# Kernel tuning notes

Hardware: AMD Instinct MI355X
Metric: run time of the kernel (lower is better)

The kernel has to match this reference:

```python
import jax, jax.numpy as jnp
import numpy as np
import math

DIMS, HEAD = 1024, 16
HD = DIMS // HEAD          # 64
B, CTX = 4, 1024
MAX_ITER, THRESH = 3, 0.5  # temp=1.0 -> q temperature scaling branch is skipped (as in torch)
LOG10_21 = math.log10(1.0 + 4000.0 / 200.0)


def _freq_angles(c):
    # compute_freqs_base: 0.2*(10**linspace(0, log10(21), d/2) - 1), custom_freqs = 36000/220 * base
    d2 = HD // 2
    mel = 10.0 ** jnp.linspace(0.0, LOG10_21, d2) - 1.0
    freqs = (36000.0 / 220.0) * (200.0 * mel / 1000.0)        # [d2]
    t = jnp.arange(c, dtype=jnp.float32)
    return t[:, None] * freqs[None, :]                          # [c, d2]


def _rope(x, ang):
    # lucidrains rotary_embedding_torch convention: interleaved pairs (x0,x1),(x2,x3),...
    x1, x2 = x[..., 0::2], x[..., 1::2]
    cos, sin = jnp.cos(ang), jnp.sin(ang)
    out = jnp.stack([x1 * cos - x2 * sin, x1 * sin + x2 * cos], axis=-1)
    return out.reshape(x.shape)


def _rms(x, w):
    eps = jnp.finfo(x.dtype).eps  # torch nn.RMSNorm eps=None default
    return x * jax.lax.rsqrt(jnp.mean(jnp.square(x), -1, keepdims=True) + eps) * w


def _sdpa(q, k, v):
    # mask is always None in this module's forward -> non-causal SDPA
    s = jnp.einsum('bhqd,bhkd->bhqk', q, k) / math.sqrt(q.shape[-1])
    return jnp.einsum('bhqk,bhkd->bhqd', jax.nn.softmax(s, -1), v)


def _focus(x, xa, P):
    # x: [b, cq, D] queries, xa: [b, ck, D] keys/values. In our configs cq == ck == eff_span.
    b, cq, D = x.shape
    ck = xa.shape[1]
    q = _rms(x, P['wq_norm']) @ P['Wq'] + P['bq']
    q = q.reshape(b, cq, HEAD, HD).transpose(0, 2, 1, 3)                 # b h c d
    kv = _rms(xa, P['wkv_norm']) @ P['Wkv'] + P['bkv']
    kv = kv.reshape(b, ck, 2, HEAD, HD).transpose(2, 0, 3, 1, 4)         # kv b h c d
    k, v = kv[0], kv[1]
    q = _rope(q, _freq_angles(cq))
    k = _rope(k, _freq_angles(ck))

    e = min(cq, ck)  # static; equals cq in all call sites here
    curq, kc, vc = q, k[:, :, :e], v[:, :, :e]
    prev = jnp.zeros_like(q)
    attn_out = jnp.zeros_like(q)
    done = jnp.asarray(False)
    for it in range(MAX_ITER):
        # torch: q/k/v re-projected from current state EVERY iteration (k,v compound)
        qp = curq[:, :, :e] @ P['Wlq'] + P['blq']
        kp = kc @ P['Wlk'] + P['blk']
        vp = vc @ P['Wlv'] + P['blv']
        attn = _sdpa(_rms(qp, P['wln']), _rms(kp, P['wln']), vp)         # == iter_out since e == cq
        diff = jnp.mean(jnp.abs(attn - prev))
        stop = (diff < THRESH) & (it > 0) & (~done)
        attn_out = jnp.where(done, attn_out, attn)  # on the break iteration attn_out = iter_out
        done = done | stop
        curq = jnp.where(done, curq, curq + attn)
        prev = jnp.where(done, prev, attn)
        kc = jnp.where(done, kc, kp)
        vc = jnp.where(done, vc, vp)
    return attn_out.transpose(0, 2, 1, 3).reshape(b, cq, D)             # b c (h d)


def _slide(x, P):
    # win_size = head_dim; only the first win_size keys of each span are ever used
    b, ctx, D = x.shape
    w = HD
    off = w // HEAD                       # span_len - win_size
    nwin = ctx // w                       # ctx chosen as a multiple of w
    starts = jnp.maximum(jnp.arange(nwin) * w - off, 0)
    kidx = starts[:, None] + jnp.arange(w)[None, :]                      # [nwin, w]
    qwin = x.reshape(b, nwin, w, D).transpose(1, 0, 2, 3)                # [nwin, b, w, D]
    kwin = x[:, kidx, :].transpose(1, 0, 2, 3)                           # [nwin, b, w, D]
    outw = jax.vmap(lambda xq, xk: _focus(xq, xk, P))(qwin, kwin)
    return outw.transpose(1, 0, 2, 3).reshape(b, ctx, D)


def _forward(x, xa, P):
    xw = _slide(x, P)
    xaw = _slide(xa, P)
    out = _focus(xw, xaw, P)
    return out @ P['Wo'] + P['bo']        # Dropout(0.01) is identity in eval


def setup_inputs() -> dict:
    key = jax.random.key(0)
    ks = jax.random.split(key, 8)
    s = 0.02
    f32 = jnp.float32
    return {
        'x': jax.random.normal(ks[0], (B, CTX, DIMS), f32),
        'xa': jax.random.normal(ks[1], (B, CTX, DIMS), f32),
        'wq_norm': jnp.ones((DIMS,), f32),
        'Wq': jax.random.normal(ks[2], (DIMS, DIMS), f32) * s,
        'bq': jnp.zeros((DIMS,), f32),
        'wkv_norm': jnp.ones((DIMS,), f32),
        'Wkv': jax.random.normal(ks[3], (DIMS, 2 * DIMS), f32) * s,
        'bkv': jnp.zeros((2 * DIMS,), f32),
        'wln': jnp.ones((HD,), f32),
        'Wlq': jax.random.normal(ks[4], (HD, HD), f32) * s,
        'blq': jnp.zeros((HD,), f32),
        'Wlk': jax.random.normal(ks[5], (HD, HD), f32) * s,
        'blk': jnp.zeros((HD,), f32),
        'Wlv': jax.random.normal(ks[6], (HD, HD), f32) * s,
        'blv': jnp.zeros((HD,), f32),
        'Wo': jax.random.normal(ks[7], (DIMS, DIMS), f32) * s,
        'bo': jnp.zeros((DIMS,), f32),
    }


def reference(x, xa, wq_norm, Wq, bq, wkv_norm, Wkv, bkv, wln, Wlq, blq, Wlk, blk, Wlv, blv, Wo, bo):
    P = dict(wq_norm=wq_norm, Wq=Wq, bq=bq, wkv_norm=wkv_norm, Wkv=Wkv, bkv=bkv, wln=wln,
             Wlq=Wlq, blq=blq, Wlk=Wlk, blk=blk, Wlv=Wlv, blv=blv, Wo=Wo, bo=bo)
    return _forward(x, xa, P)
```

## Files before the change

kernel.cpp:

```cpp
#include <hip/hip_runtime.h>
#include <math.h>

#define TPB 256

static __device__ __forceinline__ float4 mk4(float a, float b, float c, float d) {
  float4 r; r.x = a; r.y = b; r.z = c; r.w = d; return r;
}

__global__ __launch_bounds__(TPB) void k_tables(float* __restrict__ cosb,
                                                float* __restrict__ sinb) {
  int gid = blockIdx.x * TPB + threadIdx.x;
  if (gid >= 1024 * 32) return;
  int t = gid >> 5, j = gid & 31;
  const double Ld = 1.3222192947339193;
  float Lf = (float)Ld;
  float mlog;
  if (j == 31) {
    mlog = Lf;
  } else {
    float stepf = (float)((double)j / 31.0);
    mlog = (float)((double)Lf * (double)stepf);
  }
  float p = (float)pow(10.0, (double)mlog);
  float mel = p - 1.0f;
  float t2 = (200.0f * mel) / 1000.0f;
  float freq = 163.63636363636363f * t2;
  float ang = (float)t * freq;
  double a = (double)ang;
  cosb[gid] = (float)cos(a);
  sinb[gid] = (float)sin(a);
}

__global__ __launch_bounds__(TPB) void k_rowinv(const float* __restrict__ X,
                                                float* __restrict__ inv) {
  __shared__ float red[4];
  int row = blockIdx.x;
  int tid = threadIdx.x;
  float4 v = *(const float4*)(X + (size_t)row * 1024 + tid * 4);
  float ss = v.x * v.x + v.y * v.y + v.z * v.z + v.w * v.w;
#pragma unroll
  for (int m = 1; m < 64; m <<= 1) ss += __shfl_xor(ss, m);
  if ((tid & 63) == 0) red[tid >> 6] = ss;
  __syncthreads();
  if (tid == 0) {
    float s = ((red[0] + red[1]) + (red[2] + red[3]));
    float mm = s * (1.0f / 1024.0f) + 1.1920928955078125e-7f;
    inv[row] = (float)(1.0 / sqrt((double)mm));
  }
}

__global__ __launch_bounds__(TPB) void k_gemm128(
    const float* __restrict__ X, const float* __restrict__ inv,
    const float* __restrict__ wn, const float* __restrict__ W,
    const float* __restrict__ bias, float* __restrict__ o0,
    float* __restrict__ o1, int N, int mode) {
  __shared__ float As[16][132];
  __shared__ float Bs[16][132];
  int tid = threadIdx.x;
  int bx = blockIdx.x, by = blockIdx.y;
  int tx = tid & 15, ty = tid >> 4;
  float c[8][8];
#pragma unroll
  for (int i = 0; i < 8; ++i)
#pragma unroll
    for (int j = 0; j < 8; ++j) c[i][j] = 0.0f;

  int arow = tid >> 1;
  float sA = 1.0f;
  if (inv) sA = inv[by * 128 + arow];
  const float* Xrow = X + (size_t)(by * 128 + arow) * 1024;

  for (int k0 = 0; k0 < 1024; k0 += 16) {
#pragma unroll
    for (int u = 0; u < 2; ++u) {
      int kq = ((tid & 1) * 2 + u) * 4;
      float4 a4 = *(const float4*)(Xrow + k0 + kq);
      if (wn) {
        float4 w4 = *(const float4*)(wn + k0 + kq);
        a4.x *= w4.x; a4.y *= w4.y; a4.z *= w4.z; a4.w *= w4.w;
      }
      a4.x *= sA; a4.y *= sA; a4.z *= sA; a4.w *= sA;
      As[kq + 0][arow] = a4.x;
      As[kq + 1][arow] = a4.y;
      As[kq + 2][arow] = a4.z;
      As[kq + 3][arow] = a4.w;
    }
#pragma unroll
    for (int u = 0; u < 2; ++u) {
      int kr = tid >> 4;
      int c4 = ((tid & 15) * 2 + u) * 4;
      *(float4*)&Bs[kr][c4] =
          *(const float4*)(W + (size_t)(k0 + kr) * N + bx * 128 + c4);
    }
    __syncthreads();
#pragma unroll
    for (int kk = 0; kk < 16; ++kk) {
      float4 a0 = *(const float4*)&As[kk][ty * 4];
      float4 a1 = *(const float4*)&As[kk][64 + ty * 4];
      float4 b0 = *(const float4*)&Bs[kk][tx * 4];
      float4 b1 = *(const float4*)&Bs[kk][64 + tx * 4];
      float av[8] = {a0.x, a0.y, a0.z, a0.w, a1.x, a1.y, a1.z, a1.w};
      float bv[8] = {b0.x, b0.y, b0.z, b0.w, b1.x, b1.y, b1.z, b1.w};
#pragma unroll
      for (int i = 0; i < 8; ++i)
#pragma unroll
        for (int j = 0; j < 8; ++j) c[i][j] += av[i] * bv[j];
    }
    __syncthreads();
  }

#pragma unroll
  for (int jh = 0; jh < 2; ++jh) {
    int colbase = bx * 128 + jh * 64 + tx * 4;
    float4 bb = {0.f, 0.f, 0.f, 0.f};
    if (bias) bb = *(const float4*)(bias + colbase);
#pragma unroll
    for (int ih = 0; ih < 2; ++ih) {
#pragma unroll
      for (int i2 = 0; i2 < 4; ++i2) {
        int row = by * 128 + ih * 64 + ty * 4 + i2;
        int ci = ih * 4 + i2;
        float4 o;
        o.x = c[ci][jh * 4 + 0] + bb.x;
        o.y = c[ci][jh * 4 + 1] + bb.y;
        o.z = c[ci][jh * 4 + 2] + bb.z;
        o.w = c[ci][jh * 4 + 3] + bb.w;
        if (mode == 0) {
          *(float4*)(o0 + (size_t)row * N + colbase) = o;
        } else {
          int b = row >> 10, t = row & 1023;
          float* dst = o0;
          int cc = colbase;
          if (mode == 2 && colbase >= 1024) { dst = o1; cc = colbase - 1024; }
          int ch = cc >> 6, d = cc & 63;
          *(float4*)(dst + ((size_t)((b * 16 + ch) * 1024 + t)) * 64 + d) = o;
        }
      }
    }
  }
}

__global__ __launch_bounds__(TPB) void k_rope(float* __restrict__ A, int mask,
                                              const float* __restrict__ cosb,
                                              const float* __restrict__ sinb) {
  int gid = blockIdx.x * TPB + threadIdx.x;
  int j = gid & 31;
  int row = gid >> 5;
  int t = row & 1023;
  int aidx = ((t & mask) << 5) + j;
  float cc = cosb[aidx], sn = sinb[aidx];
  size_t base = (size_t)row * 64;
  float x1 = A[base + 2 * j], x2 = A[base + 2 * j + 1];
  A[base + 2 * j] = x1 * cc - x2 * sn;
  A[base + 2 * j + 1] = x1 * sn + x2 * cc;
}

__global__ __launch_bounds__(TPB) void k_gather(
    const float* __restrict__ K, const float* __restrict__ V,
    float* __restrict__ kc, float* __restrict__ vc,
    const float* __restrict__ cosb, const float* __restrict__ sinb) {
  int gid = blockIdx.x * TPB + threadIdx.x;
  int j = gid & 31;
  int tl = (gid >> 5) & 63;
  int win = (gid >> 11) & 15;
  int h = (gid >> 15) & 15;
  int b = gid >> 19;
  int sw = win * 64 - 4;
  if (win == 0) sw = 0;
  size_t bh = (size_t)(b * 16 + h) * 1024;
  size_t src = (bh + sw + tl) * 64;
  size_t dst = (bh + win * 64 + tl) * 64;
  int aidx = (tl << 5) + j;
  float cc = cosb[aidx], sn = sinb[aidx];
  float k1 = K[src + 2 * j], k2 = K[src + 2 * j + 1];
  kc[dst + 2 * j] = k1 * cc - k2 * sn;
  kc[dst + 2 * j + 1] = k1 * sn + k2 * cc;
  vc[dst + 2 * j] = V[src + 2 * j];
  vc[dst + 2 * j + 1] = V[src + 2 * j + 1];
}

__global__ __launch_bounds__(TPB) void k_proj(
    const float* __restrict__ curq, float* __restrict__ kc,
    float* __restrict__ vc, float* __restrict__ qph, float* __restrict__ kphT,
    const float* __restrict__ Wlq, const float* __restrict__ blq,
    const float* __restrict__ Wlk, const float* __restrict__ blk,
    const float* __restrict__ Wlv, const float* __restrict__ blv,
    const float* __restrict__ wln, int CQ, const int* __restrict__ flags) {
  int RT = CQ >> 4;
  int bid = blockIdx.x;
  int rt = bid % RT;
  int rest = bid / RT;
  int h = rest & 15; rest >>= 4;
  int b = rest & 3;
  int win = rest >> 2;
  if (flags && flags[win]) return;
  __shared__ float qs[16][68], ksm[16][68], vsm[16][68];
  __shared__ float Wqs[4096], Wks[4096], Wvs[4096];
  int tid = threadIdx.x;
#pragma unroll
  for (int i = 0; i < 4; ++i) {
    int f4 = (i * 256 + tid) * 4;
    *(float4*)&Wqs[f4] = *(const float4*)(Wlq + f4);
    *(float4*)&Wks[f4] = *(const float4*)(Wlk + f4);
    *(float4*)&Wvs[f4] = *(const float4*)(Wlv + f4);
  }
  int lr = tid >> 4, c4 = (tid & 15) * 4;
  int bh = b * 16 + h;
  size_t rowbase = (size_t)bh * 1024 + (size_t)win * CQ + rt * 16;
  size_t g = (rowbase + lr) * 64 + c4;
  *(float4*)&qs[lr][c4] = *(const float4*)(curq + g);
  *(float4*)&ksm[lr][c4] = *(const float4*)(kc + g);
  *(float4*)&vsm[lr][c4] = *(const float4*)(vc + g);
  __syncthreads();
  int r = tid >> 4, cg = tid & 15;
  int tglob = win * CQ + rt * 16 + r;
  const float eps = 1.1920928955078125e-7f;
  float4 wl4 = *(const float4*)(wln + cg * 4);
  size_t orow = (rowbase + r) * 64 + cg * 4;
  float4 acc;
  float ssum, rms;
  acc = *(const float4*)(blq + cg * 4);
#pragma unroll 8
  for (int k = 0; k < 64; ++k) {
    float xv = qs[r][k];
    float4 w4 = *(const float4*)&Wqs[k * 64 + cg * 4];
    acc.x += xv * w4.x; acc.y += xv * w4.y;
    acc.z += xv * w4.z; acc.w += xv * w4.w;
  }
  ssum = acc.x * acc.x + acc.y * acc.y + acc.z * acc.z + acc.w * acc.w;
#pragma unroll
  for (int m = 1; m < 16; m <<= 1) ssum += __shfl_xor(ssum, m);
  rms = (float)(1.0 / sqrt((double)(ssum * 0.015625f + eps)));
  {
    float4 o;
    o.x = acc.x * rms * wl4.x; o.y = acc.y * rms * wl4.y;
    o.z = acc.z * rms * wl4.z; o.w = acc.w * rms * wl4.w;
    *(float4*)(qph + orow) = o;
  }
  acc = *(const float4*)(blk + cg * 4);
#pragma unroll 8
  for (int k = 0; k < 64; ++k) {
    float xv = ksm[r][k];
    float4 w4 = *(const float4*)&Wks[k * 64 + cg * 4];
    acc.x += xv * w4.x; acc.y += xv * w4.y;
    acc.z += xv * w4.z; acc.w += xv * w4.w;
  }
  *(float4*)(kc + orow) = acc;
  ssum = acc.x * acc.x + acc.y * acc.y + acc.z * acc.z + acc.w * acc.w;
#pragma unroll
  for (int m = 1; m < 16; m <<= 1) ssum += __shfl_xor(ssum, m);
  rms = (float)(1.0 / sqrt((double)(ssum * 0.015625f + eps)));
  {
    float no0 = acc.x * rms * wl4.x;
    float no1 = acc.y * rms * wl4.y;
    float no2 = acc.z * rms * wl4.z;
    float no3 = acc.w * rms * wl4.w;
    size_t tb = (size_t)bh * 64 + cg * 4;
    kphT[(tb + 0) * 1024 + tglob] = no0;
    kphT[(tb + 1) * 1024 + tglob] = no1;
    kphT[(tb + 2) * 1024 + tglob] = no2;
    kphT[(tb + 3) * 1024 + tglob] = no3;
  }
  acc = *(const float4*)(blv + cg * 4);
#pragma unroll 8
  for (int k = 0; k < 64; ++k) {
    float xv = vsm[r][k];
    float4 w4 = *(const float4*)&Wvs[k * 64 + cg * 4];
    acc.x += xv * w4.x; acc.y += xv * w4.y;
    acc.z += xv * w4.z; acc.w += xv * w4.w;
  }
  *(float4*)(vc + orow) = acc;
}

template <int FRAG>
__global__ __launch_bounds__(TPB, 2) void k_attn_t(
    const float* __restrict__ qph, const float* __restrict__ kphT,
    const float* __restrict__ vbuf, float* __restrict__ curq,
    float* __restrict__ prevb, float* __restrict__ outb,
    float* __restrict__ diffp, const int* __restrict__ flags, int NQT,
    int nt, int mode) {
  constexpr int QT = FRAG * 16;
  int bid = blockIdx.x;
  int qt = bid % NQT;
  int bh = bid / NQT;
  int h = bh & 15, b = bh >> 4;
  if (mode == 2 && flags[(nt == 1) ? qt : 0]) return;
  __shared__ float qTs[64][QT];
  __shared__ float kps[64 * QT];
  __shared__ float vss[64 * 64];
  int tid = threadIdx.x;
  int tx = tid & 15, ty = tid >> 4;
  size_t bh1024 = (size_t)bh * 1024;
  size_t bh64 = (size_t)bh * 64;
  int q0 = qt * QT;
#pragma unroll
  for (int i = 0; i < FRAG; ++i) {
    int f4id = i * 256 + tid;
    int row = f4id >> 4;
    int c4 = (f4id & 15) * 4;
    float4 v = *(const float4*)(qph + (bh1024 + q0 + row) * 64 + c4);
    qTs[c4 + 0][row] = v.x;
    qTs[c4 + 1][row] = v.y;
    qTs[c4 + 2][row] = v.z;
    qTs[c4 + 3][row] = v.w;
  }
  float m[FRAG], l[FRAG], acc[FRAG][4];
#pragma unroll
  for (int i = 0; i < FRAG; ++i) {
    m[i] = -INFINITY; l[i] = 0.0f;
    acc[i][0] = acc[i][1] = acc[i][2] = acc[i][3] = 0.0f;
  }
  int kstart = (nt == 1) ? q0 : 0;
  const float SCL = 0.18033688011112042f;

  for (int kt = 0; kt < nt; ++kt) {
    int k0 = kstart + kt * 64;
#pragma unroll
    for (int i = 0; i < 4; ++i) {
      int f4id = i * 256 + tid;
      int rr = f4id >> 4;
      int c4 = (f4id & 15) * 4;
      *(float4*)&kps[rr * QT + c4] =
          *(const float4*)(kphT + (bh64 + rr) * 1024 + k0 + c4);
      *(float4*)&vss[rr * 64 + c4] =
          *(const float4*)(vbuf + (bh1024 + k0 + rr) * 64 + c4);
    }
    __syncthreads();
    float s[FRAG][4];
#pragma unroll
    for (int i = 0; i < FRAG; ++i)
      s[i][0] = s[i][1] = s[i][2] = s[i][3] = 0.0f;
#pragma unroll 4
    for (int d = 0; d < 64; ++d) {
      float4 kv = *(const float4*)&kps[d * QT + tx * 4];
      float4 qa0 = *(const float4*)&qTs[d][ty * FRAG];
      float qv[FRAG];
      qv[0] = qa0.x; qv[1] = qa0.y; qv[2] = qa0.z; qv[3] = qa0.w;
      if (FRAG == 8) {
        float4 qa1 = *(const float4*)&qTs[d][ty * FRAG + 4];
        qv[4] = qa1.x; qv[5] = qa1.y; qv[6] = qa1.z; qv[7] = qa1.w;
      }
#pragma unroll
      for (int i = 0; i < FRAG; ++i) {
        s[i][0] += qv[i] * kv.x;
        s[i][1] += qv[i] * kv.y;
        s[i][2] += qv[i] * kv.z;
        s[i][3] += qv[i] * kv.w;
      }
    }
#pragma unroll
    for (int i = 0; i < FRAG; ++i) {
      s[i][0] *= SCL; s[i][1] *= SCL; s[i][2] *= SCL; s[i][3] *= SCL;
      float r0 = fmaxf(fmaxf(s[i][0], s[i][1]), fmaxf(s[i][2], s[i][3]));
#pragma unroll
      for (int mm = 1; mm < 16; mm <<= 1) r0 = fmaxf(r0, __shfl_xor(r0, mm));
      float mnew = fmaxf(m[i], r0);
      float sc = exp2f(m[i] - mnew);
      float rs = 0.0f;
#pragma unroll
      for (int j = 0; j < 4; ++j) {
        float pv = exp2f(s[i][j] - mnew);
        s[i][j] = pv;
        rs += pv;
      }
#pragma unroll
      for (int mm = 1; mm < 16; mm <<= 1) rs += __shfl_xor(rs, mm);
      l[i] = l[i] * sc + rs;
      m[i] = mnew;
      acc[i][0] *= sc; acc[i][1] *= sc; acc[i][2] *= sc; acc[i][3] *= sc;
    }
    __syncthreads();
#pragma unroll
    for (int jj = 0; jj < 4; ++jj) {
      *(float4*)&kps[(tx * 4 + jj) * QT + ty * FRAG] =
          mk4(s[0][jj], s[1][jj], s[2][jj], s[3][jj]);
      if (FRAG == 8)
        *(float4*)&kps[(tx * 4 + jj) * QT + ty * FRAG + 4] =
            mk4(s[4][jj], s[5][jj], s[6][jj], s[7][jj]);
    }
    __syncthreads();
#pragma unroll 4
    for (int k = 0; k < 64; ++k) {
      float4 vv = *(const float4*)&vss[k * 64 + tx * 4];
      float4 pa0 = *(const float4*)&kps[k * QT + ty * FRAG];
      float pv[FRAG];
      pv[0] = pa0.x; pv[1] = pa0.y; pv[2] = pa0.z; pv[3] = pa0.w;
      if (FRAG == 8) {
        float4 pa1 = *(const float4*)&kps[k * QT + ty * FRAG + 4];
        pv[4] = pa1.x; pv[5] = pa1.y; pv[6] = pa1.z; pv[7] = pa1.w;
      }
#pragma unroll
      for (int i = 0; i < FRAG; ++i) {
        acc[i][0] += pv[i] * vv.x;
        acc[i][1] += pv[i] * vv.y;
        acc[i][2] += pv[i] * vv.z;
        acc[i][3] += pv[i] * vv.w;
      }
    }
    __syncthreads();
  }
  float ds = 0.0f;
#pragma unroll
  for (int i = 0; i < FRAG; ++i) {
    int t = q0 + ty * FRAG + i;
    float4 att;
    att.x = acc[i][0] / l[i];
    att.y = acc[i][1] / l[i];
    att.z = acc[i][2] / l[i];
    att.w = acc[i][3] / l[i];
    size_t base = (bh1024 + t) * 64 + tx * 4;
    size_t obase = ((size_t)b * 1024 + t) * 1024 + h * 64 + tx * 4;
    if (mode == 0) {
      *(float4*)(prevb + base) = att;
      float4 cq = *(const float4*)(curq + base);
      cq.x += att.x; cq.y += att.y; cq.z += att.z; cq.w += att.w;
      *(float4*)(curq + base) = cq;
    } else if (mode == 1) {
      float4 pv = *(const float4*)(prevb + base);
      ds += fabsf(att.x - pv.x) + fabsf(att.y - pv.y) +
            fabsf(att.z - pv.z) + fabsf(att.w - pv.w);
      float4 cq = *(const float4*)(curq + base);
      cq.x += att.x; cq.y += att.y; cq.z += att.z; cq.w += att.w;
      *(float4*)(curq + base) = cq;
      *(float4*)(outb + obase) = att;
    } else {
      *(float4*)(outb + obase) = att;
    }
  }
  if (mode == 1) {
    float* red = vss;
    red[tid] = ds;
    __syncthreads();
    for (int s2 = 128; s2 > 0; s2 >>= 1) {
      if (tid < s2) red[tid] += red[tid + s2];
      __syncthreads();
    }
    if (tid == 0) diffp[bid] = red[0];
  }
}

__global__ __launch_bounds__(64) void k_finalize(const float* __restrict__ diffp,
                                                 int* __restrict__ flags,
                                                 int nwin, int nper,
                                                 float count) {
  int w = threadIdx.x;
  if (w < nwin) {
    float s = 0.0f;
    for (int i = 0; i < nper; ++i) s += diffp[w + i * nwin];
    flags[w] = (s / count < 0.5f) ? 1 : 0;
  }
}

extern "C" void kernel_launch(void* const* d_in, const int* in_sizes, int n_in,
                              void* d_out, int out_size, void* d_ws,
                              size_t ws_size, hipStream_t stream) {
  const float* x = (const float*)d_in[0];
  const float* xa = (const float*)d_in[1];
  const float* wqn = (const float*)d_in[2];
  const float* Wq = (const float*)d_in[3];
  const float* bq = (const float*)d_in[4];
  const float* wkvn = (const float*)d_in[5];
  const float* Wkv = (const float*)d_in[6];
  const float* bkv = (const float*)d_in[7];
  const float* wln = (const float*)d_in[8];
  const float* Wlq = (const float*)d_in[9];
  const float* blq = (const float*)d_in[10];
  const float* Wlk = (const float*)d_in[11];
  const float* blk = (const float*)d_in[12];
  const float* Wlv = (const float*)d_in[13];
  const float* blv = (const float*)d_in[14];
  const float* Wo = (const float*)d_in[15];
  const float* bo = (const float*)d_in[16];

  float* ws = (float*)d_ws;
  const size_t SLOT = (size_t)4 * 16 * 1024 * 64;
  float* xw = ws;
  float* xaw = ws + SLOT;
  float* Q = ws + 2 * SLOT;
  float* K = ws + 3 * SLOT;
  float* V = ws + 4 * SLOT;
  float* kc = ws + 5 * SLOT;
  float* vc = ws + 6 * SLOT;
  float* prev = ws + 7 * SLOT;
  float* qph = ws + 8 * SLOT;
  float* kphT = ws + 9 * SLOT;
  float* misc = ws + 10 * SLOT;
  float* inv = misc;
  float* cosb = misc + 8192;
  float* sinb = cosb + 32768;
  float* diffp = sinb + 32768;
  int* flags = (int*)(diffp + 4096);

  k_tables<<<128, TPB, 0, stream>>>(cosb, sinb);

  for (int sl = 0; sl < 2; ++sl) {
    const float* Xin = sl ? xa : x;
    float* Xout = sl ? xaw : xw;
    k_rowinv<<<4096, TPB, 0, stream>>>(Xin, inv);
    k_gemm128<<<dim3(8, 32), TPB, 0, stream>>>(Xin, inv, wqn, Wq, bq, Q, nullptr, 1024, 1);
    k_gemm128<<<dim3(16, 32), TPB, 0, stream>>>(Xin, inv, wkvn, Wkv, bkv, K, V, 2048, 2);
    k_rope<<<8192, TPB, 0, stream>>>(Q, 63, cosb, sinb);
    k_gather<<<8192, TPB, 0, stream>>>(K, V, kc, vc, cosb, sinb);
    k_proj<<<4096, TPB, 0, stream>>>(Q, kc, vc, qph, kphT, Wlq, blq, Wlk, blk, Wlv, blv, wln, 64, nullptr);
    k_attn_t<4><<<1024, TPB, 0, stream>>>(qph, kphT, vc, Q, prev, Xout, diffp, nullptr, 16, 1, 0);
    k_proj<<<4096, TPB, 0, stream>>>(Q, kc, vc, qph, kphT, Wlq, blq, Wlk, blk, Wlv, blv, wln, 64, nullptr);
    k_attn_t<4><<<1024, TPB, 0, stream>>>(qph, kphT, vc, Q, prev, Xout, diffp, nullptr, 16, 1, 1);
    k_finalize<<<1, 64, 0, stream>>>(diffp, flags, 16, 64, 262144.0f);
    k_proj<<<4096, TPB, 0, stream>>>(Q, kc, vc, qph, kphT, Wlq, blq, Wlk, blk, Wlv, blv, wln, 64, flags);
    k_attn_t<4><<<1024, TPB, 0, stream>>>(qph, kphT, vc, Q, prev, Xout, diffp, flags, 16, 1, 2);
  }

  k_rowinv<<<4096, TPB, 0, stream>>>(xw, inv);
  k_gemm128<<<dim3(8, 32), TPB, 0, stream>>>(xw, inv, wqn, Wq, bq, Q, nullptr, 1024, 1);
  k_rowinv<<<4096, TPB, 0, stream>>>(xaw, inv);
  k_gemm128<<<dim3(16, 32), TPB, 0, stream>>>(xaw, inv, wkvn, Wkv, bkv, K, V, 2048, 2);
  k_rope<<<8192, TPB, 0, stream>>>(Q, 1023, cosb, sinb);
  k_rope<<<8192, TPB, 0, stream>>>(K, 1023, cosb, sinb);
  float* fout = xw;
  k_proj<<<4096, TPB, 0, stream>>>(Q, K, V, qph, kphT, Wlq, blq, Wlk, blk, Wlv, blv, wln, 1024, nullptr);
  k_attn_t<8><<<512, TPB, 0, stream>>>(qph, kphT, V, Q, prev, fout, diffp, nullptr, 8, 16, 0);
  k_proj<<<4096, TPB, 0, stream>>>(Q, K, V, qph, kphT, Wlq, blq, Wlk, blk, Wlv, blv, wln, 1024, nullptr);
  k_attn_t<8><<<512, TPB, 0, stream>>>(qph, kphT, V, Q, prev, fout, diffp, nullptr, 8, 16, 1);
  k_finalize<<<1, 64, 0, stream>>>(diffp, flags, 1, 512, 4194304.0f);
  k_proj<<<4096, TPB, 0, stream>>>(Q, K, V, qph, kphT, Wlq, blq, Wlk, blk, Wlv, blv, wln, 1024, flags);
  k_attn_t<8><<<512, TPB, 0, stream>>>(qph, kphT, V, Q, prev, fout, diffp, flags, 8, 16, 2);

  k_gemm128<<<dim3(8, 32), TPB, 0, stream>>>(fout, nullptr, nullptr, Wo, bo, (float*)d_out, nullptr, 1024, 0);
}
```

Measured before the change: 2.598 ms.

## Store projected keys row-major and use XOR-swizzled shared tiles in attention

The projection kernel now writes normalized keys row-major with coalesced float4 stores, replacing the strided transposed scatter into kphT. The attention kernel loads Q, K and V tiles row-major into shared memory with an XOR swizzle to avoid bank conflicts. It computes dot products as float4 along the head dimension and reuses the Q tile buffer for the probability matrix, which removes a separate transposed write and one barrier. Q is now reloaded every key tile, and the __launch_bounds__ min-blocks hint of 2 is dropped, which may change register allocation and occupancy.

```diff
diff --git a/kernel.cpp b/kernel.cpp
--- a/kernel.cpp
+++ b/kernel.cpp
@@ -181,7 +181,7 @@
 
 __global__ __launch_bounds__(TPB) void k_proj(
     const float* __restrict__ curq, float* __restrict__ kc,
-    float* __restrict__ vc, float* __restrict__ qph, float* __restrict__ kphT,
+    float* __restrict__ vc, float* __restrict__ qph, float* __restrict__ kph,
     const float* __restrict__ Wlq, const float* __restrict__ blq,
     const float* __restrict__ Wlk, const float* __restrict__ blk,
     const float* __restrict__ Wlv, const float* __restrict__ blv,
@@ -213,7 +213,6 @@
   *(float4*)&vsm[lr][c4] = *(const float4*)(vc + g);
   __syncthreads();
   int r = tid >> 4, cg = tid & 15;
-  int tglob = win * CQ + rt * 16 + r;
   const float eps = 1.1920928955078125e-7f;
   float4 wl4 = *(const float4*)(wln + cg * 4);
   size_t orow = (rowbase + r) * 64 + cg * 4;
@@ -251,15 +250,10 @@
   for (int m = 1; m < 16; m <<= 1) ssum += __shfl_xor(ssum, m);
   rms = (float)(1.0 / sqrt((double)(ssum * 0.015625f + eps)));
   {
-    float no0 = acc.x * rms * wl4.x;
-    float no1 = acc.y * rms * wl4.y;
-    float no2 = acc.z * rms * wl4.z;
-    float no3 = acc.w * rms * wl4.w;
-    size_t tb = (size_t)bh * 64 + cg * 4;
-    kphT[(tb + 0) * 1024 + tglob] = no0;
-    kphT[(tb + 1) * 1024 + tglob] = no1;
-    kphT[(tb + 2) * 1024 + tglob] = no2;
-    kphT[(tb + 3) * 1024 + tglob] = no3;
+    float4 o;
+    o.x = acc.x * rms * wl4.x; o.y = acc.y * rms * wl4.y;
+    o.z = acc.z * rms * wl4.z; o.w = acc.w * rms * wl4.w;
+    *(float4*)(kph + orow) = o;
   }
   acc = *(const float4*)(blv + cg * 4);
 #pragma unroll 8
@@ -273,37 +267,32 @@
 }
 
 template <int FRAG>
-__global__ __launch_bounds__(TPB, 2) void k_attn_t(
-    const float* __restrict__ qph, const float* __restrict__ kphT,
+__global__ __launch_bounds__(TPB) void k_attn2(
+    const float* __restrict__ qph, const float* __restrict__ kph,
     const float* __restrict__ vbuf, float* __restrict__ curq,
     float* __restrict__ prevb, float* __restrict__ outb,
     float* __restrict__ diffp, const int* __restrict__ flags, int NQT,
     int nt, int mode) {
   constexpr int QT = FRAG * 16;
+  constexpr int RS = (FRAG == 8) ? 3 : 2;
   int bid = blockIdx.x;
   int qt = bid % NQT;
   int bh = bid / NQT;
   int h = bh & 15, b = bh >> 4;
   if (mode == 2 && flags[(nt == 1) ? qt : 0]) return;
-  __shared__ float qTs[64][QT];
-  __shared__ float kps[64 * QT];
-  __shared__ float vss[64 * 64];
+  __shared__ float sQP[QT * 64];
+  __shared__ float sK[64 * 64];
+  __shared__ float sV[64 * 64];
   int tid = threadIdx.x;
   int tx = tid & 15, ty = tid >> 4;
   size_t bh1024 = (size_t)bh * 1024;
-  size_t bh64 = (size_t)bh * 64;
   int q0 = qt * QT;
-#pragma unroll
-  for (int i = 0; i < FRAG; ++i) {
-    int f4id = i * 256 + tid;
-    int row = f4id >> 4;
-    int c4 = (f4id & 15) * 4;
-    float4 v = *(const float4*)(qph + (bh1024 + q0 + row) * 64 + c4);
-    qTs[c4 + 0][row] = v.x;
-    qTs[c4 + 1][row] = v.y;
-    qTs[c4 + 2][row] = v.z;
-    qTs[c4 + 3][row] = v.w;
-  }
+  int qb[FRAG], kb[4];
+#pragma unroll
+  for (int i = 0; i < FRAG; ++i) qb[i] = (ty * FRAG + i) << 6;
+#pragma unroll
+  for (int j = 0; j < 4; ++j) kb[j] = (tx * 4 + j) << 6;
+
   float m[FRAG], l[FRAG], acc[FRAG][4];
 #pragma unroll
   for (int i = 0; i < FRAG; ++i) {
@@ -316,36 +305,46 @@
   for (int kt = 0; kt < nt; ++kt) {
     int k0 = kstart + kt * 64;
 #pragma unroll
-    for (int i = 0; i < 4; ++i) {
-      int f4id = i * 256 + tid;
-      int rr = f4id >> 4;
-      int c4 = (f4id & 15) * 4;
-      *(float4*)&kps[rr * QT + c4] =
-          *(const float4*)(kphT + (bh64 + rr) * 1024 + k0 + c4);
-      *(float4*)&vss[rr * 64 + c4] =
-          *(const float4*)(vbuf + (bh1024 + k0 + rr) * 64 + c4);
+    for (int u = 0; u < FRAG; ++u) {
+      int f4 = u * 256 + tid;
+      int row = f4 >> 4, ch = f4 & 15;
+      int cp = ((ch ^ (row >> RS)) & 15) << 2;
+      *(float4*)&sQP[(row << 6) + cp] =
+          *(const float4*)(qph + (bh1024 + q0 + row) * 64 + (ch << 2));
+    }
+#pragma unroll
+    for (int u = 0; u < 4; ++u) {
+      int f4 = u * 256 + tid;
+      int row = f4 >> 4, ch = f4 & 15;
+      int cp = ((ch ^ (row >> 2)) & 15) << 2;
+      *(float4*)&sK[(row << 6) + cp] =
+          *(const float4*)(kph + (bh1024 + k0 + row) * 64 + (ch << 2));
+      *(float4*)&sV[(row << 6) + cp] =
+          *(const float4*)(vbuf + (bh1024 + k0 + row) * 64 + (ch << 2));
     }
     __syncthreads();
+
     float s[FRAG][4];
 #pragma unroll
     for (int i = 0; i < FRAG; ++i)
       s[i][0] = s[i][1] = s[i][2] = s[i][3] = 0.0f;
-#pragma unroll 4
-    for (int d = 0; d < 64; ++d) {
-      float4 kv = *(const float4*)&kps[d * QT + tx * 4];
-      float4 qa0 = *(const float4*)&qTs[d][ty * FRAG];
-      float qv[FRAG];
-      qv[0] = qa0.x; qv[1] = qa0.y; qv[2] = qa0.z; qv[3] = qa0.w;
-      if (FRAG == 8) {
-        float4 qa1 = *(const float4*)&qTs[d][ty * FRAG + 4];
-        qv[4] = qa1.x; qv[5] = qa1.y; qv[6] = qa1.z; qv[7] = qa1.w;
-      }
+#pragma unroll 2
+    for (int d4 = 0; d4 < 16; ++d4) {
+      int kcp = ((d4 ^ tx) & 15) << 2;
+      float4 k4[4];
+#pragma unroll
+      for (int j = 0; j < 4; ++j) k4[j] = *(const float4*)&sK[kb[j] + kcp];
+      int qcp = ((d4 ^ ty) & 15) << 2;
 #pragma unroll
       for (int i = 0; i < FRAG; ++i) {
-        s[i][0] += qv[i] * kv.x;
-        s[i][1] += qv[i] * kv.y;
-        s[i][2] += qv[i] * kv.z;
-        s[i][3] += qv[i] * kv.w;
+        float4 q4 = *(const float4*)&sQP[qb[i] + qcp];
+#pragma unroll
+        for (int j = 0; j < 4; ++j) {
+          s[i][j] += q4.x * k4[j].x;
+          s[i][j] += q4.y * k4[j].y;
+          s[i][j] += q4.z * k4[j].z;
+          s[i][j] += q4.w * k4[j].w;
+        }
       }
     }
 #pragma unroll
@@ -369,32 +368,31 @@
       m[i] = mnew;
       acc[i][0] *= sc; acc[i][1] *= sc; acc[i][2] *= sc; acc[i][3] *= sc;
     }
-    __syncthreads();
-#pragma unroll
-    for (int jj = 0; jj < 4; ++jj) {
-      *(float4*)&kps[(tx * 4 + jj) * QT + ty * FRAG] =
-          mk4(s[0][jj], s[1][jj], s[2][jj], s[3][jj]);
-      if (FRAG == 8)
-        *(float4*)&kps[(tx * 4 + jj) * QT + ty * FRAG + 4] =
-            mk4(s[4][jj], s[5][jj], s[6][jj], s[7][jj]);
-    }
-    __syncthreads();
-#pragma unroll 4
-    for (int k = 0; k < 64; ++k) {
-      float4 vv = *(const float4*)&vss[k * 64 + tx * 4];
-      float4 pa0 = *(const float4*)&kps[k * QT + ty * FRAG];
-      float pv[FRAG];
-      pv[0] = pa0.x; pv[1] = pa0.y; pv[2] = pa0.z; pv[3] = pa0.w;
-      if (FRAG == 8) {
-        float4 pa1 = *(const float4*)&kps[k * QT + ty * FRAG + 4];
-        pv[4] = pa1.x; pv[5] = pa1.y; pv[6] = pa1.z; pv[7] = pa1.w;
-      }
+    {
+      int pcw = ((tx ^ ty) & 15) << 2;
+#pragma unroll
+      for (int i = 0; i < FRAG; ++i)
+        *(float4*)&sQP[qb[i] + pcw] = mk4(s[i][0], s[i][1], s[i][2], s[i][3]);
+    }
+#pragma unroll 2
+    for (int k4 = 0; k4 < 16; ++k4) {
+      int vcp = ((k4 ^ tx) & 15) << 2;
+      float4 v4[4];
+#pragma unroll
+      for (int kk = 0; kk < 4; ++kk)
+        v4[kk] = *(const float4*)&sV[((k4 * 4 + kk) << 6) + vcp];
+      int pcp = ((k4 ^ ty) & 15) << 2;
 #pragma unroll
       for (int i = 0; i < FRAG; ++i) {
-        acc[i][0] += pv[i] * vv.x;
-        acc[i][1] += pv[i] * vv.y;
-        acc[i][2] += pv[i] * vv.z;
-        acc[i][3] += pv[i] * vv.w;
+        float4 p4 = *(const float4*)&sQP[qb[i] + pcp];
+        acc[i][0] += p4.x * v4[0].x; acc[i][1] += p4.x * v4[0].y;
+        acc[i][2] += p4.x * v4[0].z; acc[i][3] += p4.x * v4[0].w;
+        acc[i][0] += p4.y * v4[1].x; acc[i][1] += p4.y * v4[1].y;
+        acc[i][2] += p4.y * v4[1].z; acc[i][3] += p4.y * v4[1].w;
+        acc[i][0] += p4.z * v4[2].x; acc[i][1] += p4.z * v4[2].y;
+        acc[i][2] += p4.z * v4[2].z; acc[i][3] += p4.z * v4[2].w;
+        acc[i][0] += p4.w * v4[3].x; acc[i][1] += p4.w * v4[3].y;
+        acc[i][2] += p4.w * v4[3].z; acc[i][3] += p4.w * v4[3].w;
       }
     }
     __syncthreads();
@@ -428,7 +426,7 @@
     }
   }
   if (mode == 1) {
-    float* red = vss;
+    float* red = sK;
     red[tid] = ds;
     __syncthreads();
     for (int s2 = 128; s2 > 0; s2 >>= 1) {
@@ -483,7 +481,7 @@
   float* vc = ws + 6 * SLOT;
   float* prev = ws + 7 * SLOT;
   float* qph = ws + 8 * SLOT;
-  float* kphT = ws + 9 * SLOT;
+  float* kph = ws + 9 * SLOT;
   float* misc = ws + 10 * SLOT;
   float* inv = misc;
   float* cosb = misc + 8192;
@@ -501,13 +499,13 @@
     k_gemm128<<<dim3(16, 32), TPB, 0, stream>>>(Xin, inv, wkvn, Wkv, bkv, K, V, 2048, 2);
     k_rope<<<8192, TPB, 0, stream>>>(Q, 63, cosb, sinb);
     k_gather<<<8192, TPB, 0, stream>>>(K, V, kc, vc, cosb, sinb);
-    k_proj<<<4096, TPB, 0, stream>>>(Q, kc, vc, qph, kphT, Wlq, blq, Wlk, blk, Wlv, blv, wln, 64, nullptr);
-    k_attn_t<4><<<1024, TPB, 0, stream>>>(qph, kphT, vc, Q, prev, Xout, diffp, nullptr, 16, 1, 0);
-    k_proj<<<4096, TPB, 0, stream>>>(Q, kc, vc, qph, kphT, Wlq, blq, Wlk, blk, Wlv, blv, wln, 64, nullptr);
-    k_attn_t<4><<<1024, TPB, 0, stream>>>(qph, kphT, vc, Q, prev, Xout, diffp, nullptr, 16, 1, 1);
+    k_proj<<<4096, TPB, 0, stream>>>(Q, kc, vc, qph, kph, Wlq, blq, Wlk, blk, Wlv, blv, wln, 64, nullptr);
+    k_attn2<4><<<1024, TPB, 0, stream>>>(qph, kph, vc, Q, prev, Xout, diffp, nullptr, 16, 1, 0);
+    k_proj<<<4096, TPB, 0, stream>>>(Q, kc, vc, qph, kph, Wlq, blq, Wlk, blk, Wlv, blv, wln, 64, nullptr);
+    k_attn2<4><<<1024, TPB, 0, stream>>>(qph, kph, vc, Q, prev, Xout, diffp, nullptr, 16, 1, 1);
     k_finalize<<<1, 64, 0, stream>>>(diffp, flags, 16, 64, 262144.0f);
-    k_proj<<<4096, TPB, 0, stream>>>(Q, kc, vc, qph, kphT, Wlq, blq, Wlk, blk, Wlv, blv, wln, 64, flags);
-    k_attn_t<4><<<1024, TPB, 0, stream>>>(qph, kphT, vc, Q, prev, Xout, diffp, flags, 16, 1, 2);
+    k_proj<<<4096, TPB, 0, stream>>>(Q, kc, vc, qph, kph, Wlq, blq, Wlk, blk, Wlv, blv, wln, 64, flags);
+    k_attn2<4><<<1024, TPB, 0, stream>>>(qph, kph, vc, Q, prev, Xout, diffp, flags, 16, 1, 2);
   }
 
   k_rowinv<<<4096, TPB, 0, stream>>>(xw, inv);
@@ -517,13 +515,13 @@
   k_rope<<<8192, TPB, 0, stream>>>(Q, 1023, cosb, sinb);
   k_rope<<<8192, TPB, 0, stream>>>(K, 1023, cosb, sinb);
   float* fout = xw;
-  k_proj<<<4096, TPB, 0, stream>>>(Q, K, V, qph, kphT, Wlq, blq, Wlk, blk, Wlv, blv, wln, 1024, nullptr);
-  k_attn_t<8><<<512, TPB, 0, stream>>>(qph, kphT, V, Q, prev, fout, diffp, nullptr, 8, 16, 0);
-  k_proj<<<4096, TPB, 0, stream>>>(Q, K, V, qph, kphT, Wlq, blq, Wlk, blk, Wlv, blv, wln, 1024, nullptr);
-  k_attn_t<8><<<512, TPB, 0, stream>>>(qph, kphT, V, Q, prev, fout, diffp, nullptr, 8, 16, 1);
+  k_proj<<<4096, TPB, 0, stream>>>(Q, K, V, qph, kph, Wlq, blq, Wlk, blk, Wlv, blv, wln, 1024, nullptr);
+  k_attn2<8><<<512, TPB, 0, stream>>>(qph, kph, V, Q, prev, fout, diffp, nullptr, 8, 16, 0);
+  k_proj<<<4096, TPB, 0, stream>>>(Q, K, V, qph, kph, Wlq, blq, Wlk, blk, Wlv, blv, wln, 1024, nullptr);
+  k_attn2<8><<<512, TPB, 0, stream>>>(qph, kph, V, Q, prev, fout, diffp, nullptr, 8, 16, 1);
   k_finalize<<<1, 64, 0, stream>>>(diffp, flags, 1, 512, 4194304.0f);
-  k_proj<<<4096, TPB, 0, stream>>>(Q, K, V, qph, kphT, Wlq, blq, Wlk, blk, Wlv, blv, wln, 1024, flags);
-  k_attn_t<8><<<512, TPB, 0, stream>>>(qph, kphT, V, Q, prev, fout, diffp, flags, 8, 16, 2);
+  k_proj<<<4096, TPB, 0, stream>>>(Q, K, V, qph, kph, Wlq, blq, Wlk, blk, Wlv, blv, wln, 1024, flags);
+  k_attn2<8><<<512, TPB, 0, stream>>>(qph, kph, V, Q, prev, fout, diffp, flags, 8, 16, 2);
 
   k_gemm128<<<dim3(8, 32), TPB, 0, stream>>>(fout, nullptr, nullptr, Wo, bo, (float*)d_out, nullptr, 1024, 0);
 }
```

New measurement: 2.657 ms. 1.02x slower.
